# Kernel tuning notes

Hardware: AMD Instinct MI355X
Metric: run time of the kernel (lower is better)

## Reference

```python
import jax, jax.numpy as jnp
import numpy as np

B, N, M, C = 8, 76725, 32, 12  # N = 9 anchors x (80^2+40^2+20^2+10^2+5^2) for a 640x640 image, P3-P7
IMG = 640.0


def setup_inputs() -> dict:
    key = jax.random.key(0)
    ks = jax.random.split(key, 7)
    # logits biased toward prior_prob~0.01 like the head's bias init
    cls_logits = jax.random.normal(ks[0], (B, N, C), jnp.float32) - 4.0
    box_deltas = 0.1 * jax.random.normal(ks[1], (B, N, 4), jnp.float32)
    # plausible anchors: random centers in image, sizes 16..256
    a_xy = jax.random.uniform(ks[2], (N, 2), jnp.float32) * IMG
    a_wh = 16.0 + jax.random.uniform(ks[3], (N, 2), jnp.float32) * 240.0
    anchors = jnp.concatenate([a_xy - 0.5 * a_wh, a_xy + 0.5 * a_wh], axis=-1)
    # padded ground truth: M boxes per image, all valid
    g_xy = jax.random.uniform(ks[4], (B, M, 2), jnp.float32) * (IMG - 96.0)
    g_wh = 16.0 + jax.random.uniform(ks[5], (B, M, 2), jnp.float32) * 80.0
    gt_boxes = jnp.concatenate([g_xy, g_xy + g_wh], axis=-1)
    gt_labels = jax.random.randint(ks[6], (B, M), 0, C)
    gt_valid = jnp.ones((B, M), dtype=bool)
    return {"cls_logits": cls_logits, "box_deltas": box_deltas, "anchors": anchors,
            "gt_boxes": gt_boxes, "gt_labels": gt_labels, "gt_valid": gt_valid}


def _box_iou(anchors, gt_boxes):
    # anchors [N,4], gt_boxes [B,M,4] -> [B,N,M]
    ax1, ay1, ax2, ay2 = (anchors[:, i] for i in range(4))
    gx1, gy1, gx2, gy2 = (gt_boxes[..., i] for i in range(4))
    iw = jnp.clip(jnp.minimum(ax2[None, :, None], gx2[:, None, :])
                  - jnp.maximum(ax1[None, :, None], gx1[:, None, :]), 0.0)
    ih = jnp.clip(jnp.minimum(ay2[None, :, None], gy2[:, None, :])
                  - jnp.maximum(ay1[None, :, None], gy1[:, None, :]), 0.0)
    inter = iw * ih
    area_a = (ax2 - ax1) * (ay2 - ay1)            # [N]
    area_g = (gx2 - gx1) * (gy2 - gy1)            # [B,M]
    union = area_a[None, :, None] + area_g[:, None, :] - inter
    return inter / union


def _encode_boxes(anchors, matched):
    aw = anchors[:, 2] - anchors[:, 0]
    ah = anchors[:, 3] - anchors[:, 1]
    acx = anchors[:, 0] + 0.5 * aw
    acy = anchors[:, 1] + 0.5 * ah
    gw = matched[..., 2] - matched[..., 0]
    gh = matched[..., 3] - matched[..., 1]
    gcx = matched[..., 0] + 0.5 * gw
    gcy = matched[..., 1] + 0.5 * gh
    return jnp.stack([(gcx - acx) / aw, (gcy - acy) / ah,
                      jnp.log(gw / aw), jnp.log(gh / ah)], axis=-1)


def reference(cls_logits, box_deltas, anchors, gt_boxes, gt_labels, gt_valid):
    # --- anchor assignment (box_iou + max over GT) ---
    ious = _box_iou(anchors, gt_boxes)                       # [B,N,M]
    ious = jnp.where(gt_valid[:, None, :], ious, -1.0)
    iou_max = ious.max(axis=-1)                              # [B,N]
    idx = ious.argmax(axis=-1)                               # [B,N]
    pos = iou_max >= 0.5
    valid = pos | (iou_max < 0.4)                            # non-ignore anchors
    matched = jnp.take_along_axis(
        gt_boxes, jnp.broadcast_to(idx[:, :, None], (B, N, 4)), axis=1)  # [B,N,4]
    mlab = jnp.take_along_axis(gt_labels, idx, axis=1)       # [B,N]
    f32 = cls_logits.dtype
    cls_t = jax.nn.one_hot(mlab, C, dtype=f32) * pos[..., None].astype(f32)
    # --- sigmoid focal loss (alpha=0.25, gamma=2), mean over non-ignored elements ---
    p = jax.nn.sigmoid(cls_logits)
    ce = -(cls_t * jax.nn.log_sigmoid(cls_logits)
           + (1.0 - cls_t) * jax.nn.log_sigmoid(-cls_logits))
    pt = cls_t * p + (1.0 - cls_t) * (1.0 - p)
    alpha_t = cls_t * 0.25 + (1.0 - cls_t) * 0.75
    focal = alpha_t * (1.0 - pt) ** 2 * ce                   # [B,N,C]
    vw = valid.astype(f32)
    cls_loss = jnp.sum(focal * vw[..., None]) / jnp.maximum(jnp.sum(vw) * C, 1.0)
    # --- smooth L1 (beta=1) on positives, mean over selected elements ---
    box_t = _encode_boxes(anchors, matched)                  # [B,N,4]
    d = jnp.abs(box_deltas - box_t)
    sl1 = jnp.where(d < 1.0, 0.5 * d * d, d - 0.5)
    pw = pos.astype(f32)
    box_loss = jnp.sum(sl1 * pw[..., None]) / jnp.maximum(jnp.sum(pw) * 4.0, 1.0)
    return cls_loss + box_loss
```

## Files before the change

### kernel.cpp

```cpp
#include <hip/hip_runtime.h>
#include <math.h>

#define NB 8
#define NA 76725
#define NM 32
#define NC 12
#define BLK 256
#define CHX 300
#define NBLOCKS (CHX * NB)


__global__ __launch_bounds__(BLK, 4) void retina_main(
    const float* __restrict__ cls_logits,
    const float* __restrict__ box_deltas,
    const float* __restrict__ anchors,
    const float* __restrict__ gt_boxes,
    const int* __restrict__ gt_labels,
    char* __restrict__ ws,
    int mode, int nslots, int sstride)
{
    __shared__ float4 s_gt[NM];
    __shared__ float  s_area[NM];
    __shared__ int    s_lab[NM];
    __shared__ float4 s_red[BLK / 64];

    const int b    = blockIdx.y;
    const int tid  = threadIdx.x;
    const int n    = blockIdx.x * BLK + tid;
    const bool live = (n < NA);
    const int nc   = live ? n : (NA - 1);

    const float4 a = ((const float4*)anchors)[nc];
    const float4* clp = (const float4*)(cls_logits + ((size_t)b * NA + nc) * NC);
    const float4 c0 = clp[0], c1 = clp[1], c2 = clp[2];
    const float4 d4 = ((const float4*)box_deltas)[(size_t)b * NA + nc];

    if (tid < NM) {
        float4 g = ((const float4*)gt_boxes)[b * NM + tid];
        s_gt[tid]   = g;
        s_area[tid] = (g.z - g.x) * (g.w - g.y);
        s_lab[tid]  = gt_labels[b * NM + tid];
    }
    __syncthreads();

    const float area_a = (a.z - a.x) * (a.w - a.y);

    float bi[4], bS[4]; int bx[4];
    #pragma unroll
    for (int q = 0; q < 4; ++q) {
        const int m0 = q * 8;
        float4 g = s_gt[m0];
        float iw = fmaxf(fminf(a.z, g.z) - fmaxf(a.x, g.x), 0.0f);
        float ih = fmaxf(fminf(a.w, g.w) - fmaxf(a.y, g.y), 0.0f);
        bi[q] = iw * ih;
        bS[q] = area_a + s_area[m0];
        bx[q] = m0;
        #pragma unroll
        for (int mm = 1; mm < 8; ++mm) {
            const int m = m0 + mm;
            g  = s_gt[m];
            iw = fmaxf(fminf(a.z, g.z) - fmaxf(a.x, g.x), 0.0f);
            ih = fmaxf(fminf(a.w, g.w) - fmaxf(a.y, g.y), 0.0f);
            const float inter = iw * ih;
            const float S     = area_a + s_area[m];
            const bool gt = inter * bS[q] > bi[q] * S;
            bi[q] = gt ? inter : bi[q];
            bS[q] = gt ? S     : bS[q];
            bx[q] = gt ? m     : bx[q];
        }
    }
    float Bi = bi[0], BS = bS[0]; int Bx = bx[0];
    #pragma unroll
    for (int q = 1; q < 4; ++q) {
        const bool gt = bi[q] * BS > Bi * bS[q];
        Bi = gt ? bi[q] : Bi;
        BS = gt ? bS[q] : BS;
        Bx = gt ? bx[q] : Bx;
    }
    const float Bu = BS - Bi;

    const bool pos   = live && (Bi >= 0.5f * Bu);
    const bool valid = live && (pos || (Bi < 0.4f * Bu));

    const int lab = pos ? s_lab[Bx] : -1;
    float x[NC];
    x[0]=c0.x; x[1]=c0.y; x[2]=c0.z; x[3]=c0.w;
    x[4]=c1.x; x[5]=c1.y; x[6]=c1.z; x[7]=c1.w;
    x[8]=c2.x; x[9]=c2.y; x[10]=c2.z; x[11]=c2.w;
    float facc = 0.0f;
    #pragma unroll
    for (int c = 0; c < NC; ++c) {
        const float xx = x[c];
        const bool tgt = (c == lab);
        const float z  = tgt ? -xx : xx;
        const float e  = __expf(-fabsf(xx));
        const float t  = 1.0f + e;
        const float l  = __logf(t);
        const float u  = __builtin_amdgcn_rcpf(t);
        const float v  = e * u;
        const float q  = (z >= 0.0f) ? u : v;
        const float s  = l + fmaxf(z, 0.0f);
        const float al = tgt ? 0.25f : 0.75f;
        facc += al * (q * q) * s;
    }

    float sacc = 0.0f;
    {
        const float4 g  = s_gt[Bx];
        const float aw  = a.z - a.x;
        const float ah  = a.w - a.y;
        const float r_aw = __builtin_amdgcn_rcpf(aw);
        const float r_ah = __builtin_amdgcn_rcpf(ah);
        const float acx = a.x + 0.5f * aw;
        const float acy = a.y + 0.5f * ah;
        const float gw  = g.z - g.x;
        const float gh  = g.w - g.y;
        const float gcx = g.x + 0.5f * gw;
        const float gcy = g.y + 0.5f * gh;
        const float t0 = (gcx - acx) * r_aw;
        const float t1 = (gcy - acy) * r_ah;
        const float t2 = __logf(gw * r_aw);
        const float t3 = __logf(gh * r_ah);
        float d;
        d = fabsf(d4.x - t0); sacc += (d < 1.0f) ? 0.5f * d * d : d - 0.5f;
        d = fabsf(d4.y - t1); sacc += (d < 1.0f) ? 0.5f * d * d : d - 0.5f;
        d = fabsf(d4.z - t2); sacc += (d < 1.0f) ? 0.5f * d * d : d - 0.5f;
        d = fabsf(d4.w - t3); sacc += (d < 1.0f) ? 0.5f * d * d : d - 0.5f;
    }

    float4 v4 = make_float4(valid ? facc : 0.0f,
                            pos   ? sacc : 0.0f,
                            valid ? 1.0f : 0.0f,
                            pos   ? 1.0f : 0.0f);
    #pragma unroll
    for (int off = 32; off > 0; off >>= 1) {
        v4.x += __shfl_down(v4.x, off);
        v4.y += __shfl_down(v4.y, off);
        v4.z += __shfl_down(v4.z, off);
        v4.w += __shfl_down(v4.w, off);
    }
    const int wave = tid >> 6;
    const int lane = tid & 63;
    if (lane == 0) s_red[wave] = v4;
    __syncthreads();

    if (tid == 0) {
        float4 t = s_red[0];
        #pragma unroll
        for (int w = 1; w < BLK / 64; ++w) {
            t.x += s_red[w].x; t.y += s_red[w].y;
            t.z += s_red[w].z; t.w += s_red[w].w;
        }
        const int bid = blockIdx.y * gridDim.x + blockIdx.x;
        if (mode == 2) {
            double* p = (double*)(ws + (size_t)bid * 32);
            p[0] = (double)t.x; p[1] = (double)t.y;
            p[2] = (double)t.z; p[3] = (double)t.w;
        } else {
            double* p = (double*)(ws + (size_t)(bid & (nslots - 1)) * sstride);
            atomicAdd(&p[0], (double)t.x);
            atomicAdd(&p[1], (double)t.y);
            atomicAdd(&p[2], (double)t.z);
            atomicAdd(&p[3], (double)t.w);
        }
    }
}

__global__ __launch_bounds__(256) void retina_finalize(
    const char* __restrict__ ws, int nslots, int sstride,
    float* __restrict__ out)
{
    const int tid = threadIdx.x;
    double fs = 0.0, ss = 0.0, vc = 0.0, pc = 0.0;
    for (int i = tid; i < nslots; i += 256) {
        const double* p = (const double*)(ws + (size_t)i * sstride);
        fs += p[0]; ss += p[1]; vc += p[2]; pc += p[3];
    }
    #pragma unroll
    for (int off = 32; off > 0; off >>= 1) {
        fs += __shfl_down(fs, off);
        ss += __shfl_down(ss, off);
        vc += __shfl_down(vc, off);
        pc += __shfl_down(pc, off);
    }
    __shared__ double sred[4][4];
    const int wave = tid >> 6;
    const int lane = tid & 63;
    if (lane == 0) {
        sred[wave][0] = fs; sred[wave][1] = ss;
        sred[wave][2] = vc; sred[wave][3] = pc;
    }
    __syncthreads();
    if (tid == 0) {
        #pragma unroll
        for (int w = 1; w < 4; ++w) {
            fs += sred[w][0]; ss += sred[w][1];
            vc += sred[w][2]; pc += sred[w][3];
        }
        const double cls_loss = fs / fmax(vc * (double)NC, 1.0);
        const double box_loss = ss / fmax(pc * 4.0, 1.0);
        out[0] = (float)(cls_loss + box_loss);
    }
}

extern "C" void kernel_launch(void* const* d_in, const int* in_sizes, int n_in,
                              void* d_out, int out_size, void* d_ws, size_t ws_size,
                              hipStream_t stream) {
    const float* cls_logits = (const float*)d_in[0];
    const float* box_deltas = (const float*)d_in[1];
    const float* anchors    = (const float*)d_in[2];
    const float* gt_boxes   = (const float*)d_in[3];
    const int*   gt_labels  = (const int*)d_in[4];
    float* out = (float*)d_out;

    int mode, nslots, sstride;
    if (ws_size >= (size_t)NBLOCKS * 32)      { mode = 2; nslots = NBLOCKS; sstride = 32; }
    else if (ws_size >= (size_t)(64 * 64))    { mode = 1; nslots = 64;      sstride = 64; }
    else                                       { mode = 0; nslots = 1;       sstride = 32; }

    if (mode != 2)
        hipMemsetAsync(d_ws, 0, (size_t)nslots * sstride, stream);

    dim3 grid(CHX, NB);
    retina_main<<<grid, BLK, 0, stream>>>(
        cls_logits, box_deltas, anchors, gt_boxes, gt_labels,
        (char*)d_ws, mode, nslots, sstride);
    retina_finalize<<<1, 256, 0, stream>>>((const char*)d_ws, nslots, sstride, out);
}
```

Measured before the change: 101.9 us.

## Drop shared memory and block barriers; write per-wave partials, widen finalize

The main kernel no longer stages GT boxes, areas and labels in LDS. It reads them straight from global memory, which should hit cache as uniform loads, and recomputes GT areas inline. The block-level reduction and both __syncthreads are removed, so each wave writes its own float4 partial to the workspace. The finalize kernel grows to 1024 threads to sum the four-times-larger partial array. This trades barrier and LDS overhead for more global loads per thread, more workspace writes, and a larger serial final reduction.

```diff
diff --git a/kernel.cpp b/kernel.cpp
--- a/kernel.cpp
+++ b/kernel.cpp
@@ -8,6 +8,8 @@
 #define BLK 256
 #define CHX 300
 #define NBLOCKS (CHX * NB)
+#define WPB (BLK / 64)
+#define NWAVES (NBLOCKS * WPB)
 
 
 __global__ __launch_bounds__(BLK, 4) void retina_main(
@@ -19,11 +21,6 @@
     char* __restrict__ ws,
     int mode, int nslots, int sstride)
 {
-    __shared__ float4 s_gt[NM];
-    __shared__ float  s_area[NM];
-    __shared__ int    s_lab[NM];
-    __shared__ float4 s_red[BLK / 64];
-
     const int b    = blockIdx.y;
     const int tid  = threadIdx.x;
     const int n    = blockIdx.x * BLK + tid;
@@ -35,34 +32,29 @@
     const float4 c0 = clp[0], c1 = clp[1], c2 = clp[2];
     const float4 d4 = ((const float4*)box_deltas)[(size_t)b * NA + nc];
 
-    if (tid < NM) {
-        float4 g = ((const float4*)gt_boxes)[b * NM + tid];
-        s_gt[tid]   = g;
-        s_area[tid] = (g.z - g.x) * (g.w - g.y);
-        s_lab[tid]  = gt_labels[b * NM + tid];
-    }
-    __syncthreads();
-
     const float area_a = (a.z - a.x) * (a.w - a.y);
+    const float4* gtb = (const float4*)gt_boxes + b * NM;
 
     float bi[4], bS[4]; int bx[4];
     #pragma unroll
     for (int q = 0; q < 4; ++q) {
         const int m0 = q * 8;
-        float4 g = s_gt[m0];
-        float iw = fmaxf(fminf(a.z, g.z) - fmaxf(a.x, g.x), 0.0f);
-        float ih = fmaxf(fminf(a.w, g.w) - fmaxf(a.y, g.y), 0.0f);
-        bi[q] = iw * ih;
-        bS[q] = area_a + s_area[m0];
-        bx[q] = m0;
+        {
+            const float4 g = gtb[m0];
+            const float iw = fmaxf(fminf(a.z, g.z) - fmaxf(a.x, g.x), 0.0f);
+            const float ih = fmaxf(fminf(a.w, g.w) - fmaxf(a.y, g.y), 0.0f);
+            bi[q] = iw * ih;
+            bS[q] = area_a + (g.z - g.x) * (g.w - g.y);
+            bx[q] = m0;
+        }
         #pragma unroll
         for (int mm = 1; mm < 8; ++mm) {
             const int m = m0 + mm;
-            g  = s_gt[m];
-            iw = fmaxf(fminf(a.z, g.z) - fmaxf(a.x, g.x), 0.0f);
-            ih = fmaxf(fminf(a.w, g.w) - fmaxf(a.y, g.y), 0.0f);
+            const float4 g = gtb[m];
+            const float iw = fmaxf(fminf(a.z, g.z) - fmaxf(a.x, g.x), 0.0f);
+            const float ih = fmaxf(fminf(a.w, g.w) - fmaxf(a.y, g.y), 0.0f);
             const float inter = iw * ih;
-            const float S     = area_a + s_area[m];
+            const float S     = area_a + (g.z - g.x) * (g.w - g.y);
             const bool gt = inter * bS[q] > bi[q] * S;
             bi[q] = gt ? inter : bi[q];
             bS[q] = gt ? S     : bS[q];
@@ -82,7 +74,10 @@
     const bool pos   = live && (Bi >= 0.5f * Bu);
     const bool valid = live && (pos || (Bi < 0.4f * Bu));
 
-    const int lab = pos ? s_lab[Bx] : -1;
+    const float4 g  = ((const float4*)gt_boxes)[b * NM + Bx];
+    const int    ml = gt_labels[b * NM + Bx];
+    const int    lab = pos ? ml : -1;
+
     float x[NC];
     x[0]=c0.x; x[1]=c0.y; x[2]=c0.z; x[3]=c0.w;
     x[4]=c1.x; x[5]=c1.y; x[6]=c1.z; x[7]=c1.w;
@@ -106,7 +101,6 @@
 
     float sacc = 0.0f;
     {
-        const float4 g  = s_gt[Bx];
         const float aw  = a.z - a.x;
         const float ah  = a.w - a.y;
         const float r_aw = __builtin_amdgcn_rcpf(aw);
@@ -139,42 +133,38 @@
         v4.z += __shfl_down(v4.z, off);
         v4.w += __shfl_down(v4.w, off);
     }
-    const int wave = tid >> 6;
     const int lane = tid & 63;
-    if (lane == 0) s_red[wave] = v4;
-    __syncthreads();
-
-    if (tid == 0) {
-        float4 t = s_red[0];
-        #pragma unroll
-        for (int w = 1; w < BLK / 64; ++w) {
-            t.x += s_red[w].x; t.y += s_red[w].y;
-            t.z += s_red[w].z; t.w += s_red[w].w;
-        }
-        const int bid = blockIdx.y * gridDim.x + blockIdx.x;
-        if (mode == 2) {
-            double* p = (double*)(ws + (size_t)bid * 32);
-            p[0] = (double)t.x; p[1] = (double)t.y;
-            p[2] = (double)t.z; p[3] = (double)t.w;
+    if (lane == 0) {
+        const int wid = (b * CHX + blockIdx.x) * WPB + (tid >> 6);
+        if (mode == 3) {
+            ((float4*)ws)[wid] = v4;
         } else {
-            double* p = (double*)(ws + (size_t)(bid & (nslots - 1)) * sstride);
-            atomicAdd(&p[0], (double)t.x);
-            atomicAdd(&p[1], (double)t.y);
-            atomicAdd(&p[2], (double)t.z);
-            atomicAdd(&p[3], (double)t.w);
+            double* p = (double*)(ws + (size_t)(wid & (nslots - 1)) * sstride);
+            atomicAdd(&p[0], (double)v4.x);
+            atomicAdd(&p[1], (double)v4.y);
+            atomicAdd(&p[2], (double)v4.z);
+            atomicAdd(&p[3], (double)v4.w);
         }
     }
 }
 
-__global__ __launch_bounds__(256) void retina_finalize(
-    const char* __restrict__ ws, int nslots, int sstride,
+__global__ __launch_bounds__(1024) void retina_finalize(
+    const char* __restrict__ ws, int mode, int nslots, int sstride,
     float* __restrict__ out)
 {
     const int tid = threadIdx.x;
     double fs = 0.0, ss = 0.0, vc = 0.0, pc = 0.0;
-    for (int i = tid; i < nslots; i += 256) {
-        const double* p = (const double*)(ws + (size_t)i * sstride);
-        fs += p[0]; ss += p[1]; vc += p[2]; pc += p[3];
+    if (mode == 3) {
+        const float4* sl = (const float4*)ws;
+        for (int i = tid; i < nslots; i += 1024) {
+            const float4 v = sl[i];
+            fs += v.x; ss += v.y; vc += v.z; pc += v.w;
+        }
+    } else {
+        for (int i = tid; i < nslots; i += 1024) {
+            const double* p = (const double*)(ws + (size_t)i * sstride);
+            fs += p[0]; ss += p[1]; vc += p[2]; pc += p[3];
+        }
     }
     #pragma unroll
     for (int off = 32; off > 0; off >>= 1) {
@@ -183,7 +173,7 @@
         vc += __shfl_down(vc, off);
         pc += __shfl_down(pc, off);
     }
-    __shared__ double sred[4][4];
+    __shared__ double sred[16][4];
     const int wave = tid >> 6;
     const int lane = tid & 63;
     if (lane == 0) {
@@ -193,7 +183,7 @@
     __syncthreads();
     if (tid == 0) {
         #pragma unroll
-        for (int w = 1; w < 4; ++w) {
+        for (int w = 1; w < 16; ++w) {
             fs += sred[w][0]; ss += sred[w][1];
             vc += sred[w][2]; pc += sred[w][3];
         }
@@ -214,16 +204,17 @@
     float* out = (float*)d_out;
 
     int mode, nslots, sstride;
-    if (ws_size >= (size_t)NBLOCKS * 32)      { mode = 2; nslots = NBLOCKS; sstride = 32; }
-    else if (ws_size >= (size_t)(64 * 64))    { mode = 1; nslots = 64;      sstride = 64; }
-    else                                       { mode = 0; nslots = 1;       sstride = 32; }
-
-    if (mode != 2)
+    if (ws_size >= (size_t)NWAVES * 16)     { mode = 3; nslots = NWAVES; sstride = 16; }
+    else if (ws_size >= (size_t)(64 * 64))  { mode = 1; nslots = 64;     sstride = 64; }
+    else                                    { mode = 0; nslots = 1;      sstride = 32; }
+
+    if (mode != 3)
         hipMemsetAsync(d_ws, 0, (size_t)nslots * sstride, stream);
 
     dim3 grid(CHX, NB);
     retina_main<<<grid, BLK, 0, stream>>>(
         cls_logits, box_deltas, anchors, gt_boxes, gt_labels,
         (char*)d_ws, mode, nslots, sstride);
-    retina_finalize<<<1, 256, 0, stream>>>((const char*)d_ws, nslots, sstride, out);
+    retina_finalize<<<1, 1024, 0, stream>>>(
+        (const char*)d_ws, mode, nslots, sstride, out);
 }
```

Measured after the change: 107.6 us. 5.6% more time.
